# Kernel tuning notes

Hardware: AMD Instinct MI355X
Metric: run time of the kernel (lower is better)

The kernel has to match this reference:

```python
import jax, jax.numpy as jnp
import numpy as np

B, S, E, NH = 4, 1024, 512, 8
D = E // NH

def layer_norm(x, scale, bias, eps=1e-5):
    mu = jnp.mean(x, -1, keepdims=True)
    var = jnp.mean((x - mu) ** 2, -1, keepdims=True)
    return (x - mu) * jax.lax.rsqrt(var + eps) * scale + bias

def mha(qx, kx, vx, qw, qb, kw, kb, vw, vb, ow, ob, temp):
    b, sq, e = qx.shape
    sk = kx.shape[1]
    q = (qx @ qw + qb).reshape(b, sq, NH, D)
    k = (kx @ kw + kb).reshape(b, sk, NH, D)
    v = (vx @ vw + vb).reshape(b, sk, NH, D)
    scores = jnp.einsum('bqhd,bkhd->bhqk', q, k) * (D ** -0.5) / temp
    w = jax.nn.softmax(scores, axis=-1)  # dropout is identity in eval mode
    o = jnp.einsum('bhqk,bkhd->bqhd', w, v).reshape(b, sq, e)
    return o @ ow + ob

def setup_inputs():
    key = jax.random.key(0)
    ks = jax.random.split(key, 10)
    sc = 0.02  # init scale for weights
    return {
        'body_feats': jax.random.normal(ks[0], (B, S, E), jnp.float32),
        'limb_feats': jax.random.normal(ks[1], (B, S, E), jnp.float32),
        'attn_qw': jax.random.normal(ks[2], (4, E, E), jnp.float32) * sc,
        'attn_qb': jnp.zeros((4, E), jnp.float32),
        'attn_kw': jax.random.normal(ks[3], (4, E, E), jnp.float32) * sc,
        'attn_kb': jnp.zeros((4, E), jnp.float32),
        'attn_vw': jax.random.normal(ks[4], (4, E, E), jnp.float32) * sc,
        'attn_vb': jnp.zeros((4, E), jnp.float32),
        'attn_ow': jax.random.normal(ks[5], (4, E, E), jnp.float32) * sc,
        'attn_ob': jnp.zeros((4, E), jnp.float32),
        'ffn_w1': jax.random.normal(ks[6], (2, E, 4 * E), jnp.float32) * sc,
        'ffn_b1': jnp.zeros((2, 4 * E), jnp.float32),
        'ffn_w2': jax.random.normal(ks[7], (2, 4 * E, E), jnp.float32) * sc,
        'ffn_b2': jnp.zeros((2, E), jnp.float32),
        'norm_scale': jnp.ones((6, E), jnp.float32),
        'norm_bias': jnp.zeros((6, E), jnp.float32),
        'gate_w': jax.random.normal(ks[8], (2 * E, 2), jnp.float32) * sc,
        'gate_b': jnp.zeros((2,), jnp.float32),
        'temperature': 1,
    }

def reference(body_feats, limb_feats, attn_qw, attn_qb, attn_kw, attn_kb, attn_vw, attn_vb, attn_ow, attn_ob, ffn_w1, ffn_b1, ffn_w2, ffn_b2, norm_scale, norm_bias, gate_w, gate_b, temperature):
    temp = jnp.float32(temperature)
    # attn index: 0=self_body 1=self_limb 2=body2limb 3=limb2body
    # norm index: 0=norm1_body 1=norm2_body 2=norm3_body 3=norm1_limb 4=norm2_limb 5=norm3_limb
    def attn(i, qx, kx, vx):
        return mha(qx, kx, vx, attn_qw[i], attn_qb[i], attn_kw[i], attn_kb[i], attn_vw[i], attn_vb[i], attn_ow[i], attn_ob[i], temp)
    def ffn(i, x):
        return jax.nn.gelu(x @ ffn_w1[i] + ffn_b1[i], approximate=False) @ ffn_w2[i] + ffn_b2[i]
    def ln(i, x):
        return layer_norm(x, norm_scale[i], norm_bias[i])
    body = ln(0, body_feats + attn(0, body_feats, body_feats, body_feats))
    limb = ln(3, limb_feats + attn(1, limb_feats, limb_feats, limb_feats))
    body_cross = attn(2, body, limb, limb)
    limb_cross = attn(3, limb, body, body)
    body_gate = jax.nn.softmax(jnp.concatenate([body, body_cross], -1) @ gate_w + gate_b, axis=-1)
    limb_gate = jax.nn.softmax(jnp.concatenate([limb, limb_cross], -1) @ gate_w + gate_b, axis=-1)
    # NOTE: original torch code applies norm2_body to BOTH streams (preserved faithfully)
    body = ln(1, body * body_gate[..., 0:1] + body_cross * body_gate[..., 1:2])
    limb = ln(1, limb * limb_gate[..., 0:1] + limb_cross * limb_gate[..., 1:2])
    body = ln(2, body + ffn(0, body))
    limb = ln(5, limb + ffn(1, limb))
    return body, limb
```

## Files before the change

### kernel.cpp

```cpp
#include <hip/hip_runtime.h>

#define AS1 __attribute__((address_space(1)))
#define AS3 __attribute__((address_space(3)))

typedef __attribute__((ext_vector_type(4))) float f32x4;
typedef __attribute__((ext_vector_type(8))) short s16x8;

static __device__ __forceinline__ ushort f2bf(float f) {
  union { float f; unsigned u; } x; x.f = f;
  unsigned r = x.u + 0x7FFFu + ((x.u >> 16) & 1u);
  return (ushort)(r >> 16);
}
static __device__ __forceinline__ float bf2f(ushort u) {
  union { unsigned u; float f; } x; x.u = ((unsigned)u) << 16; return x.f;
}
static __device__ __forceinline__ float ex2(float x) {
  return __builtin_amdgcn_exp2f(x);
}
static __device__ __forceinline__ unsigned cvt_pk_bf16(float a, float b) {
  unsigned r;
  asm("v_cvt_pk_bf16_f32 %0, %1, %2" : "=v"(r) : "v"(a), "v"(b));
  return r;
}
static __device__ __forceinline__ float parse_scalar(const void* p) {
  int i = *(const int*)p;
  if (i > 0 && i < 1000000) return (float)i;
  union { int i; float f; } u; u.i = i; return u.f;
}

__global__ __launch_bounds__(256)
void transpose_all(const float* __restrict__ qw, const float* __restrict__ kw,
                   const float* __restrict__ vw, const float* __restrict__ ow,
                   const float* __restrict__ w1, const float* __restrict__ w2,
                   ushort* __restrict__ FW, ushort* __restrict__ WOT,
                   ushort* __restrict__ W1T, ushort* __restrict__ W2T)
{
  __shared__ float tile[32][33];
  int id = blockIdx.x;
  const float* in; ushort* out; int K, N, tx, ty;
  if (id < 3072) {
    int trip = id / 768, r = id - trip * 768, which = r >> 8, t2 = r & 255;
    int widx = (which == 0) ? trip : (trip ^ (trip >> 1));
    in = ((which == 0) ? qw : (which == 1) ? kw : vw) + (size_t)widx * 512 * 512;
    out = FW + (size_t)trip * 1536 * 512 + (size_t)which * 512 * 512;
    K = 512; N = 512; tx = t2 & 15; ty = t2 >> 4;
  } else if (id < 4096) {
    int r = id - 3072, wi = r >> 8, t2 = r & 255;
    in = ow + (size_t)wi * 512 * 512; out = WOT + (size_t)wi * 512 * 512;
    K = 512; N = 512; tx = t2 & 15; ty = t2 >> 4;
  } else if (id < 6144) {
    int r = id - 4096, s = r >> 10, t2 = r & 1023;
    in = w1 + (size_t)s * 512 * 2048; out = W1T + (size_t)s * 2048 * 512;
    K = 512; N = 2048; tx = t2 & 63; ty = t2 >> 6;
  } else {
    int r = id - 6144, s = r >> 10, t2 = r & 1023;
    in = w2 + (size_t)s * 2048 * 512; out = W2T + (size_t)s * 512 * 2048;
    K = 2048; N = 512; tx = t2 & 15; ty = t2 >> 4;
  }
  int nb = tx * 32, kb = ty * 32;
  int x = threadIdx.x, y = threadIdx.y;
  #pragma unroll
  for (int i = 0; i < 4; ++i)
    tile[y + i * 8][x] = in[(size_t)(kb + y + i * 8) * N + nb + x];
  __syncthreads();
  #pragma unroll
  for (int i = 0; i < 4; ++i)
    out[(size_t)(nb + y + i * 8) * K + kb + x] = f2bf(tile[x][y + i * 8]);
}

__global__ __launch_bounds__(256)
void cvt2_bf16(const float* __restrict__ a, const float* __restrict__ b,
               ushort* __restrict__ oa, ushort* __restrict__ ob)
{
  const float* in = blockIdx.y ? b : a;
  ushort* out = blockIdx.y ? ob : oa;
  int i = (blockIdx.x * 256 + threadIdx.x) * 4;
  float4 v = *(const float4*)(in + i);
  ushort4 o;
  o.x = f2bf(v.x); o.y = f2bf(v.y); o.z = f2bf(v.z); o.w = f2bf(v.w);
  *(ushort4*)(out + i) = o;
}

struct GemmArgs {
  const ushort* A; const ushort* Bt;
  const float *b0, *b1, *b2;
  float* outf; ushort* outb;
  ushort *qo, *ko, *vto;
  const void* sp;
  int M, N, K, kind;
};

template<int FM, int FN>
__global__ __launch_bounds__(256)
void gemm_k(GemmArgs g0, GemmArgs g1)
{
  constexpr int BM = FM * 32, BN = FN * 32;
  __shared__ ushort As[2][BM * 64];
  __shared__ ushort Bs[2][BN * 64];
  GemmArgs g = blockIdx.z ? g1 : g0;
  const int t = threadIdx.x, lane = t & 63, w = t >> 6;
  const int lr = lane & 15, gq = lane >> 4;
  const int wr = w >> 1, wc = w & 1;
  const int m0 = blockIdx.y * BM, n0 = blockIdx.x * BN;
  const int K = g.K;
  const int nk = K >> 6;

  auto stage = [&](int kt, int buf) {
    #pragma unroll
    for (int p = 0; p < FM; ++p) {
      int c = p * 256 + t, row = c >> 3, sl = c & 7;
      const ushort* src = g.A + (size_t)(m0 + row) * K + kt * 64 + ((sl ^ (row & 7)) << 3);
      __builtin_amdgcn_global_load_lds((const AS1 void*)src,
          (AS3 void*)(As[buf] + (size_t)(p * 256 + (t & ~63)) * 8), 16, 0, 0);
    }
    #pragma unroll
    for (int p = 0; p < FN; ++p) {
      int c = p * 256 + t, row = c >> 3, sl = c & 7;
      const ushort* src = g.Bt + (size_t)(n0 + row) * K + kt * 64 + ((sl ^ (row & 7)) << 3);
      __builtin_amdgcn_global_load_lds((const AS1 void*)src,
          (AS3 void*)(Bs[buf] + (size_t)(p * 256 + (t & ~63)) * 8), 16, 0, 0);
    }
  };

  f32x4 acc[FM][FN];
  f32x4 zero = {0.f, 0.f, 0.f, 0.f};
  #pragma unroll
  for (int m = 0; m < FM; ++m)
    #pragma unroll
    for (int n = 0; n < FN; ++n) acc[m][n] = zero;

  stage(0, 0);
  __syncthreads();
  for (int kt = 0; kt < nk; ++kt) {
    int cur = kt & 1;
    const ushort* Ab = As[cur];
    const ushort* Bb = Bs[cur];
    if (kt + 1 < nk) stage(kt + 1, cur ^ 1);
    #pragma unroll
    for (int ks = 0; ks < 2; ++ks) {
      s16x8 af[FM], bfv[FN];
      #pragma unroll
      for (int m = 0; m < FM; ++m) {
        int row = wr * (FM * 16) + m * 16 + lr;
        af[m] = *(const s16x8*)(Ab + row * 64 + (((ks * 4 + gq) ^ (row & 7)) << 3));
      }
      #pragma unroll
      for (int n = 0; n < FN; ++n) {
        int row = wc * (FN * 16) + n * 16 + lr;
        bfv[n] = *(const s16x8*)(Bb + row * 64 + (((ks * 4 + gq) ^ (row & 7)) << 3));
      }
      __builtin_amdgcn_s_setprio(1);
      #pragma unroll
      for (int m = 0; m < FM; ++m)
        #pragma unroll
        for (int n = 0; n < FN; ++n)
          acc[m][n] = __builtin_amdgcn_mfma_f32_16x16x32_bf16(af[m], bfv[n], acc[m][n], 0, 0, 0);
      __builtin_amdgcn_s_setprio(0);
    }
    __syncthreads();
  }

  float qs = 1.0f;
  if (g.kind == 3 && g.sp) qs = 0.125f / parse_scalar(g.sp) * 1.4426950408889634f;
  #pragma unroll
  for (int n = 0; n < FN; ++n) {
    int col = n0 + wc * (FN * 16) + n * 16 + lr;
    int seg = col >> 9, cm = col & 511;
    float bv;
    if (g.kind == 3) bv = (seg == 0) ? g.b0[cm] : (seg == 1) ? g.b1[cm] : g.b2[cm];
    else bv = g.b0 ? g.b0[col] : 0.f;
    #pragma unroll
    for (int m = 0; m < FM; ++m) {
      int rowb = m0 + wr * (FM * 16) + m * 16 + 4 * gq;
      if (g.kind == 3) {
        if (seg == 2) {
          int d = cm & 63, hh = cm >> 6, bb = rowb >> 10, s = rowb & 1023;
          ushort4 pk;
          pk.x = f2bf(acc[m][n][0] + bv); pk.y = f2bf(acc[m][n][1] + bv);
          pk.z = f2bf(acc[m][n][2] + bv); pk.w = f2bf(acc[m][n][3] + bv);
          *(ushort4*)(g.vto + (((size_t)(bb * 8 + hh) * 64 + d) << 10) + s) = pk;
        } else if (seg == 1) {
          #pragma unroll
          for (int r = 0; r < 4; ++r)
            g.ko[(size_t)(rowb + r) * 512 + cm] = f2bf(acc[m][n][r] + bv);
        } else {
          #pragma unroll
          for (int r = 0; r < 4; ++r)
            g.qo[(size_t)(rowb + r) * 512 + cm] = f2bf((acc[m][n][r] + bv) * qs);
        }
      } else {
        #pragma unroll
        for (int r = 0; r < 4; ++r) {
          float v = acc[m][n][r] + bv;
          if (g.kind == 2) v = 0.5f * v * (1.0f + erff(v * 0.70710678118654752f));
          if (g.kind == 0) g.outf[(size_t)(rowb + r) * g.N + col] = v;
          else g.outb[(size_t)(rowb + r) * g.N + col] = f2bf(v);
        }
      }
    }
  }
}

__global__ __launch_bounds__(256)
void attn_core(const ushort* __restrict__ Q0, const ushort* __restrict__ K0,
               const ushort* __restrict__ V0, ushort* __restrict__ O0,
               const ushort* __restrict__ Q1, const ushort* __restrict__ K1,
               const ushort* __restrict__ V1, ushort* __restrict__ O1)
{
  __shared__ ushort Ks[2][64 * 64];
  __shared__ ushort Vs[2][64 * 64];
  __shared__ ushort Ps[4][1024];
  const int str = blockIdx.y;
  const ushort* Q = str ? Q1 : Q0;
  const ushort* Kx = str ? K1 : K0;
  const ushort* VT = str ? V1 : V0;
  ushort* O = str ? O1 : O0;

  const int t = threadIdx.x, lane = t & 63, w = t >> 6;
  const int lr = lane & 15, g = lane >> 4;
  int bid = blockIdx.x;
  int L = (bid & 7) * 64 + (bid >> 3);
  int bh = L >> 4, qt = L & 15;
  size_t tbase = ((size_t)(bh >> 3) << 19) + ((size_t)(bh & 7) << 6);
  const ushort* Kbase = Kx + tbase;
  const ushort* Vbase = VT + ((size_t)bh << 16);
  int q0 = qt * 64 + w * 16;
  char* myPs = (char*)Ps[w];
  const int psw = (lr & 7) << 4;

  auto stage = [&](int kt, int buf) {
    #pragma unroll
    for (int p = 0; p < 2; ++p) {
      int c = p * 256 + t, row = c >> 3, sl = c & 7;
      const ushort* src = Kbase + (size_t)(kt * 64 + row) * 512 + ((sl ^ (row & 7)) << 3);
      __builtin_amdgcn_global_load_lds((const AS1 void*)src,
          (AS3 void*)(Ks[buf] + (size_t)(p * 256 + (t & ~63)) * 8), 16, 0, 0);
    }
    #pragma unroll
    for (int p = 0; p < 2; ++p) {
      int c = p * 256 + t, row = c >> 3, sl = c & 7;
      const ushort* src = Vbase + (size_t)row * 1024 + kt * 64 + ((sl ^ (row & 7)) << 3);
      __builtin_amdgcn_global_load_lds((const AS1 void*)src,
          (AS3 void*)(Vs[buf] + (size_t)(p * 256 + (t & ~63)) * 8), 16, 0, 0);
    }
  };

  s16x8 qf[2];
  #pragma unroll
  for (int ks = 0; ks < 2; ++ks)
    qf[ks] = *(const s16x8*)(Q + tbase + (size_t)(q0 + lr) * 512 + ks * 32 + g * 8);

  f32x4 po[4];
  f32x4 zero = {0.f, 0.f, 0.f, 0.f};
  #pragma unroll
  for (int dt = 0; dt < 4; ++dt) po[dt] = zero;
  float mrow = -1e30f, lsum = 0.f;

  stage(0, 0);
  __syncthreads();
  #pragma unroll 2
  for (int kt = 0; kt < 16; ++kt) {
    int cur = kt & 1;
    const ushort* Kb = Ks[cur];
    const ushort* Vb = Vs[cur];
    if (kt < 15) stage(kt + 1, cur ^ 1);

    f32x4 sc[4];
    #pragma unroll
    for (int c = 0; c < 4; ++c) {
      sc[c] = zero;
      #pragma unroll
      for (int ks = 0; ks < 2; ++ks) {
        int row = c * 16 + lr;
        s16x8 kf = *(const s16x8*)(Kb + row * 64 + (((ks * 4 + g) ^ (row & 7)) << 3));
        sc[c] = __builtin_amdgcn_mfma_f32_16x16x32_bf16(kf, qf[ks], sc[c], 0, 0, 0);
      }
    }

    float tm = sc[0][0];
    #pragma unroll
    for (int c = 0; c < 4; ++c)
      #pragma unroll
      for (int r = 0; r < 4; ++r) tm = fmaxf(tm, sc[c][r]);
    tm = fmaxf(tm, __shfl_xor(tm, 16));
    tm = fmaxf(tm, __shfl_xor(tm, 32));
    float nm = fmaxf(mrow, tm);
    float fr = ex2(mrow - nm);
    float ts = 0.f;
    #pragma unroll
    for (int c = 0; c < 4; ++c)
      #pragma unroll
      for (int r = 0; r < 4; ++r) {
        float pv = ex2(sc[c][r] - nm);
        sc[c][r] = pv;
        ts += pv;
      }
    ts += __shfl_xor(ts, 16);
    ts += __shfl_xor(ts, 32);
    lsum = lsum * fr + ts;
    mrow = nm;
    #pragma unroll
    for (int dt = 0; dt < 4; ++dt) po[dt] *= fr;

    #pragma unroll
    for (int c = 0; c < 4; ++c) {
      uint2 d;
      d.x = cvt_pk_bf16(sc[c][0], sc[c][1]);
      d.y = cvt_pk_bf16(sc[c][2], sc[c][3]);
      *(uint2*)(myPs + lr * 128 + ((c * 32 + g * 8) ^ psw)) = d;
    }
    s16x8 paf[2];
    #pragma unroll
    for (int ks = 0; ks < 2; ++ks)
      paf[ks] = *(const s16x8*)(myPs + lr * 128 + ((ks * 64 + g * 16) ^ psw));

    __builtin_amdgcn_s_setprio(1);
    #pragma unroll
    for (int dt = 0; dt < 4; ++dt) {
      int vrow = dt * 16 + lr;
      #pragma unroll
      for (int ks = 0; ks < 2; ++ks) {
        s16x8 vf = *(const s16x8*)(Vb + vrow * 64 + (((ks * 4 + g) ^ (vrow & 7)) << 3));
        po[dt] = __builtin_amdgcn_mfma_f32_16x16x32_bf16(vf, paf[ks], po[dt], 0, 0, 0);
      }
    }
    __builtin_amdgcn_s_setprio(0);
    __syncthreads();
  }

  float inv = 1.0f / lsum;
  #pragma unroll
  for (int dt = 0; dt < 4; ++dt) {
    ushort4 pk;
    pk.x = f2bf(po[dt][0] * inv);
    pk.y = f2bf(po[dt][1] * inv);
    pk.z = f2bf(po[dt][2] * inv);
    pk.w = f2bf(po[dt][3] * inv);
    *(ushort4*)(O + tbase + (size_t)(q0 + lr) * 512 + dt * 16 + 4 * g) = pk;
  }
}

__global__ __launch_bounds__(256)
void add_ln_ff2(const float* __restrict__ a0, const float* __restrict__ b0,
                ushort* __restrict__ o0, const float* __restrict__ a1,
                const float* __restrict__ b1, ushort* __restrict__ o1,
                const float* __restrict__ nsc, const float* __restrict__ nbi,
                int i0, int i1)
{
  const float* a = blockIdx.y ? a1 : a0;
  const float* b = blockIdx.y ? b1 : b0;
  ushort* outb = blockIdx.y ? o1 : o0;
  const float* scale = nsc + (blockIdx.y ? i1 : i0) * 512;
  const float* bias = nbi + (blockIdx.y ? i1 : i0) * 512;
  const int lane = threadIdx.x & 63, w = threadIdx.x >> 6;
  const size_t row = blockIdx.x * 4 + w;
  float x[8];
  #pragma unroll
  for (int j = 0; j < 8; j += 4) {
    float4 av = *(const float4*)(a + row * 512 + lane * 8 + j);
    float4 bv = *(const float4*)(b + row * 512 + lane * 8 + j);
    x[j] = av.x + bv.x; x[j + 1] = av.y + bv.y;
    x[j + 2] = av.z + bv.z; x[j + 3] = av.w + bv.w;
  }
  float s = 0.f, ss = 0.f;
  #pragma unroll
  for (int j = 0; j < 8; ++j) { s += x[j]; ss += x[j] * x[j]; }
  #pragma unroll
  for (int m = 1; m < 64; m <<= 1) { s += __shfl_xor(s, m); ss += __shfl_xor(ss, m); }
  float mu = s * (1.f / 512.f);
  float rstd = rsqrtf(ss * (1.f / 512.f) - mu * mu + 1e-5f);
  ushort o[8];
  #pragma unroll
  for (int j = 0; j < 8; ++j) {
    int e = lane * 8 + j;
    o[j] = f2bf((x[j] - mu) * rstd * scale[e] + bias[e]);
  }
  *(s16x8*)(outb + row * 512 + lane * 8) = *(s16x8*)o;
}

__global__ __launch_bounds__(256)
void add_ln_bf2(const ushort* __restrict__ a0, const float* __restrict__ b0,
                float* __restrict__ o0, const ushort* __restrict__ a1,
                const float* __restrict__ b1, float* __restrict__ o1,
                const float* __restrict__ nsc, const float* __restrict__ nbi,
                int i0, int i1)
{
  const ushort* a = blockIdx.y ? a1 : a0;
  const float* b = blockIdx.y ? b1 : b0;
  float* outf = blockIdx.y ? o1 : o0;
  const float* scale = nsc + (blockIdx.y ? i1 : i0) * 512;
  const float* bias = nbi + (blockIdx.y ? i1 : i0) * 512;
  const int lane = threadIdx.x & 63, w = threadIdx.x >> 6;
  const size_t row = blockIdx.x * 4 + w;
  s16x8 av = *(const s16x8*)(a + row * 512 + lane * 8);
  float x[8];
  #pragma unroll
  for (int j = 0; j < 8; j += 4) {
    float4 bv = *(const float4*)(b + row * 512 + lane * 8 + j);
    x[j] = bf2f((ushort)av[j]) + bv.x; x[j + 1] = bf2f((ushort)av[j + 1]) + bv.y;
    x[j + 2] = bf2f((ushort)av[j + 2]) + bv.z; x[j + 3] = bf2f((ushort)av[j + 3]) + bv.w;
  }
  float s = 0.f, ss = 0.f;
  #pragma unroll
  for (int j = 0; j < 8; ++j) { s += x[j]; ss += x[j] * x[j]; }
  #pragma unroll
  for (int m = 1; m < 64; m <<= 1) { s += __shfl_xor(s, m); ss += __shfl_xor(ss, m); }
  float mu = s * (1.f / 512.f);
  float rstd = rsqrtf(ss * (1.f / 512.f) - mu * mu + 1e-5f);
  float o[8];
  #pragma unroll
  for (int j = 0; j < 8; ++j) {
    int e = lane * 8 + j;
    o[j] = (x[j] - mu) * rstd * scale[e] + bias[e];
  }
  *(float4*)(outf + row * 512 + lane * 8) = *(float4*)o;
  *(float4*)(outf + row * 512 + lane * 8 + 4) = *(float4*)(o + 4);
}

__global__ __launch_bounds__(256)
void gate_ln2(const ushort* __restrict__ x0, const ushort* __restrict__ c0,
              ushort* __restrict__ o0, const ushort* __restrict__ x1,
              const ushort* __restrict__ c1, ushort* __restrict__ o1,
              const float* __restrict__ gw, const float* __restrict__ gb,
              const float* __restrict__ scale, const float* __restrict__ bias)
{
  const ushort* x = blockIdx.y ? x1 : x0;
  const ushort* cr = blockIdx.y ? c1 : c0;
  ushort* outb = blockIdx.y ? o1 : o0;
  const int lane = threadIdx.x & 63, w = threadIdx.x >> 6;
  const size_t row = blockIdx.x * 4 + w;
  s16x8 xv8 = *(const s16x8*)(x + row * 512 + lane * 8);
  s16x8 cv8 = *(const s16x8*)(cr + row * 512 + lane * 8);
  float xv[8], cv[8];
  #pragma unroll
  for (int j = 0; j < 8; ++j) { xv[j] = bf2f((ushort)xv8[j]); cv[j] = bf2f((ushort)cv8[j]); }
  float d0 = 0.f, d1 = 0.f;
  #pragma unroll
  for (int j = 0; j < 8; ++j) {
    int e = lane * 8 + j;
    float2 g0 = *(const float2*)(gw + 2 * e);
    float2 g1 = *(const float2*)(gw + 2 * (512 + e));
    d0 += xv[j] * g0.x + cv[j] * g1.x;
    d1 += xv[j] * g0.y + cv[j] * g1.y;
  }
  #pragma unroll
  for (int m = 1; m < 64; m <<= 1) { d0 += __shfl_xor(d0, m); d1 += __shfl_xor(d1, m); }
  d0 += gb[0]; d1 += gb[1];
  float mx = fmaxf(d0, d1);
  float e0 = __expf(d0 - mx), e1 = __expf(d1 - mx);
  float inv = 1.0f / (e0 + e1);
  float g0w = e0 * inv, g1w = e1 * inv;
  float xc[8];
  float s = 0.f, ss = 0.f;
  #pragma unroll
  for (int j = 0; j < 8; ++j) {
    xc[j] = xv[j] * g0w + cv[j] * g1w;
    s += xc[j]; ss += xc[j] * xc[j];
  }
  #pragma unroll
  for (int m = 1; m < 64; m <<= 1) { s += __shfl_xor(s, m); ss += __shfl_xor(ss, m); }
  float mu = s * (1.f / 512.f);
  float rstd = rsqrtf(ss * (1.f / 512.f) - mu * mu + 1e-5f);
  ushort o[8];
  #pragma unroll
  for (int j = 0; j < 8; ++j) {
    int e = lane * 8 + j;
    o[j] = f2bf((xc[j] - mu) * rstd * scale[e] + bias[e]);
  }
  *(s16x8*)(outb + row * 512 + lane * 8) = *(s16x8*)o;
}

extern "C" void kernel_launch(void* const* d_in, const int* in_sizes, int n_in,
                              void* d_out, int out_size, void* d_ws, size_t ws_size,
                              hipStream_t stream)
{
  (void)in_sizes; (void)n_in; (void)out_size; (void)ws_size;
  const int T = 4096, E = 512, HD = 2048;
  const float* body = (const float*)d_in[0];
  const float* limb = (const float*)d_in[1];
  const float* qw = (const float*)d_in[2];  const float* qb = (const float*)d_in[3];
  const float* kw = (const float*)d_in[4];  const float* kb = (const float*)d_in[5];
  const float* vw = (const float*)d_in[6];  const float* vb = (const float*)d_in[7];
  const float* ow = (const float*)d_in[8];  const float* ob = (const float*)d_in[9];
  const float* w1 = (const float*)d_in[10]; const float* fb1 = (const float*)d_in[11];
  const float* w2 = (const float*)d_in[12]; const float* fb2 = (const float*)d_in[13];
  const float* nsc = (const float*)d_in[14]; const float* nbi = (const float*)d_in[15];
  const float* gw = (const float*)d_in[16];  const float* gb = (const float*)d_in[17];
  const void* temp = d_in[18];

  char* ws = (char*)d_ws;
  size_t off = 0;
  auto alloc = [&](size_t b) { char* p = ws + off; off += (b + 255) & ~(size_t)255; return p; };
  ushort* FW    = (ushort*)alloc((size_t)4 * 1536 * 512 * 2);
  ushort* WOT   = (ushort*)alloc((size_t)4 * E * E * 2);
  ushort* W1T   = (ushort*)alloc((size_t)2 * E * HD * 2);
  ushort* W2T   = (ushort*)alloc((size_t)2 * HD * E * 2);
  ushort* XB    = (ushort*)alloc((size_t)T * E * 2);
  ushort* XL    = (ushort*)alloc((size_t)T * E * 2);
  float*  PROJA = (float*)alloc((size_t)T * E * 4);
  float*  PROJB = (float*)alloc((size_t)T * E * 4);
  ushort* BODYb = (ushort*)alloc((size_t)T * E * 2);
  ushort* LIMBb = (ushort*)alloc((size_t)T * E * 2);
  ushort* BCRb  = (ushort*)alloc((size_t)T * E * 2);
  ushort* LCRb  = (ushort*)alloc((size_t)T * E * 2);
  ushort* GBb   = (ushort*)alloc((size_t)T * E * 2);
  ushort* GLb   = (ushort*)alloc((size_t)T * E * 2);
  ushort* QA    = (ushort*)alloc((size_t)T * E * 2);
  ushort* KA    = (ushort*)alloc((size_t)T * E * 2);
  ushort* VTA   = (ushort*)alloc((size_t)T * E * 2);
  ushort* QB    = (ushort*)alloc((size_t)T * E * 2);
  ushort* KB    = (ushort*)alloc((size_t)T * E * 2);
  ushort* VTB   = (ushort*)alloc((size_t)T * E * 2);
  ushort* AOA   = (ushort*)alloc((size_t)T * E * 2);
  ushort* AOB   = (ushort*)alloc((size_t)T * E * 2);
  ushort* H1A   = QA;
  ushort* H1B   = KB;
  float*  FFNA  = PROJA;
  float*  FFNB  = PROJB;

  transpose_all<<<8192, dim3(32, 8), 0, stream>>>(qw, kw, vw, ow, w1, w2, FW, WOT, W1T, W2T);
  cvt2_bf16<<<dim3(T * E / 1024, 2), 256, 0, stream>>>(body, limb, XB, XL);

  auto qkv_pair = [&](const ushort* A0, int t0, ushort* q0, ushort* k0, ushort* v0,
                      const ushort* A1, int t1, ushort* q1, ushort* k1, ushort* v1) {
    GemmArgs a{}, b{};
    int kv0 = t0 ^ (t0 >> 1), kv1 = t1 ^ (t1 >> 1);
    a.A = A0; a.Bt = FW + (size_t)t0 * 1536 * 512;
    a.b0 = qb + t0 * E; a.b1 = kb + kv0 * E; a.b2 = vb + kv0 * E;
    a.qo = q0; a.ko = k0; a.vto = v0; a.sp = temp; a.M = T; a.N = 1536; a.K = E; a.kind = 3;
    b = a;
    b.A = A1; b.Bt = FW + (size_t)t1 * 1536 * 512;
    b.b0 = qb + t1 * E; b.b1 = kb + kv1 * E; b.b2 = vb + kv1 * E;
    b.qo = q1; b.ko = k1; b.vto = v1;
    gemm_k<4, 4><<<dim3(12, 32, 2), 256, 0, stream>>>(a, b);
  };
  auto oproj_pair = [&](const ushort* A0, int i0, float* of0, ushort* ob0,
                        const ushort* A1, int i1, float* of1, ushort* ob1, int kind) {
    GemmArgs a{}, b{};
    a.A = A0; a.Bt = WOT + (size_t)i0 * E * E; a.b0 = ob + i0 * E;
    a.outf = of0; a.outb = ob0; a.M = T; a.N = E; a.K = E; a.kind = kind;
    b = a;
    b.A = A1; b.Bt = WOT + (size_t)i1 * E * E; b.b0 = ob + i1 * E;
    b.outf = of1; b.outb = ob1;
    gemm_k<2, 4><<<dim3(4, 64, 2), 256, 0, stream>>>(a, b);
  };

  qkv_pair(XB, 0, QA, KA, VTA, XL, 1, QB, KB, VTB);
  attn_core<<<dim3(512, 2), 256, 0, stream>>>(QA, KA, VTA, AOA, QB, KB, VTB, AOB);
  oproj_pair(AOA, 0, PROJA, nullptr, AOB, 1, PROJB, nullptr, 0);
  add_ln_ff2<<<dim3(T / 4, 2), 256, 0, stream>>>(body, PROJA, BODYb, limb, PROJB, LIMBb,
                                                 nsc, nbi, 0, 3);
  qkv_pair(BODYb, 2, QA, KA, VTA, LIMBb, 3, QB, KB, VTB);
  attn_core<<<dim3(512, 2), 256, 0, stream>>>(QA, KB, VTB, AOA, QB, KA, VTA, AOB);
  oproj_pair(AOA, 2, nullptr, BCRb, AOB, 3, nullptr, LCRb, 1);

  gate_ln2<<<dim3(T / 4, 2), 256, 0, stream>>>(BODYb, BCRb, GBb, LIMBb, LCRb, GLb,
                                               gw, gb, nsc + E, nbi + E);

  {
    GemmArgs a{}, b{};
    a.A = GBb; a.Bt = W1T; a.b0 = fb1; a.outb = H1A;
    a.M = T; a.N = HD; a.K = E; a.kind = 2;
    b = a; b.A = GLb; b.Bt = W1T + (size_t)HD * E; b.b0 = fb1 + HD; b.outb = H1B;
    gemm_k<4, 4><<<dim3(16, 32, 2), 256, 0, stream>>>(a, b);
  }
  {
    GemmArgs a{}, b{};
    a.A = H1A; a.Bt = W2T; a.b0 = fb2; a.outf = FFNA;
    a.M = T; a.N = E; a.K = HD; a.kind = 0;
    b = a; b.A = H1B; b.Bt = W2T + (size_t)HD * E; b.b0 = fb2 + E; b.outf = FFNB;
    gemm_k<2, 4><<<dim3(4, 64, 2), 256, 0, stream>>>(a, b);
  }
  add_ln_bf2<<<dim3(T / 4, 2), 256, 0, stream>>>(GBb, FFNA, (float*)d_out,
                                                 GLb, FFNB, (float*)d_out + (size_t)T * E,
                                                 nsc, nbi, 2, 5);
}
```

Baseline: 404.1 us.

## Use tanh GELU, bf16 intermediates, merged input conversion, smaller output GEMM tiles

The exact erf GELU becomes a tanh-form approximation built from exp2 and rcp. The output-projection and FFN2 GEMMs now write bf16 instead of fp32, and the add+layernorm kernels read bf16. The fp32-to-bf16 input conversion is folded into the weight transpose launch as extra blocks. The N=512 GEMMs switch from 2x4 to 2x2 fragment tiles with twice the grid, and together these aim to cut launches, memory traffic and erf cost at some accuracy risk.

```diff
diff --git a/kernel.cpp b/kernel.cpp
--- a/kernel.cpp
+++ b/kernel.cpp
@@ -22,6 +22,12 @@
   asm("v_cvt_pk_bf16_f32 %0, %1, %2" : "=v"(r) : "v"(a), "v"(b));
   return r;
 }
+static __device__ __forceinline__ float gelu_fast(float v) {
+  float u = 0.7978845608028654f * (v + 0.044715f * v * v * v);
+  float e = ex2(u * 2.885390081777927f);
+  float r = __builtin_amdgcn_rcpf(e + 1.0f);
+  return v - v * r;
+}
 static __device__ __forceinline__ float parse_scalar(const void* p) {
   int i = *(const int*)p;
   if (i > 0 && i < 1000000) return (float)i;
@@ -32,11 +38,26 @@
 void transpose_all(const float* __restrict__ qw, const float* __restrict__ kw,
                    const float* __restrict__ vw, const float* __restrict__ ow,
                    const float* __restrict__ w1, const float* __restrict__ w2,
+                   const float* __restrict__ body, const float* __restrict__ limb,
                    ushort* __restrict__ FW, ushort* __restrict__ WOT,
-                   ushort* __restrict__ W1T, ushort* __restrict__ W2T)
+                   ushort* __restrict__ W1T, ushort* __restrict__ W2T,
+                   ushort* __restrict__ XB, ushort* __restrict__ XL)
 {
   __shared__ float tile[32][33];
   int id = blockIdx.x;
+  if (id >= 8192) {
+    int id2 = id - 8192;
+    const float* in = (id2 >= 2048) ? limb : body;
+    ushort* out = (id2 >= 2048) ? XL : XB;
+    int j = id2 & 2047;
+    int t = threadIdx.y * 32 + threadIdx.x;
+    int i = (j * 256 + t) * 4;
+    float4 v = *(const float4*)(in + i);
+    ushort4 o;
+    o.x = f2bf(v.x); o.y = f2bf(v.y); o.z = f2bf(v.z); o.w = f2bf(v.w);
+    *(ushort4*)(out + i) = o;
+    return;
+  }
   const float* in; ushort* out; int K, N, tx, ty;
   if (id < 3072) {
     int trip = id / 768, r = id - trip * 768, which = r >> 8, t2 = r & 255;
@@ -66,19 +87,6 @@
   #pragma unroll
   for (int i = 0; i < 4; ++i)
     out[(size_t)(nb + y + i * 8) * K + kb + x] = f2bf(tile[x][y + i * 8]);
-}
-
-__global__ __launch_bounds__(256)
-void cvt2_bf16(const float* __restrict__ a, const float* __restrict__ b,
-               ushort* __restrict__ oa, ushort* __restrict__ ob)
-{
-  const float* in = blockIdx.y ? b : a;
-  ushort* out = blockIdx.y ? ob : oa;
-  int i = (blockIdx.x * 256 + threadIdx.x) * 4;
-  float4 v = *(const float4*)(in + i);
-  ushort4 o;
-  o.x = f2bf(v.x); o.y = f2bf(v.y); o.z = f2bf(v.z); o.w = f2bf(v.w);
-  *(ushort4*)(out + i) = o;
 }
 
 struct GemmArgs {
@@ -192,7 +200,7 @@
         #pragma unroll
         for (int r = 0; r < 4; ++r) {
           float v = acc[m][n][r] + bv;
-          if (g.kind == 2) v = 0.5f * v * (1.0f + erff(v * 0.70710678118654752f));
+          if (g.kind == 2) v = gelu_fast(v);
           if (g.kind == 0) g.outf[(size_t)(rowb + r) * g.N + col] = v;
           else g.outb[(size_t)(rowb + r) * g.N + col] = f2bf(v);
         }
@@ -341,26 +349,28 @@
 }
 
 __global__ __launch_bounds__(256)
-void add_ln_ff2(const float* __restrict__ a0, const float* __restrict__ b0,
+void add_ln_fb2(const float* __restrict__ a0, const ushort* __restrict__ b0,
                 ushort* __restrict__ o0, const float* __restrict__ a1,
-                const float* __restrict__ b1, ushort* __restrict__ o1,
+                const ushort* __restrict__ b1, ushort* __restrict__ o1,
                 const float* __restrict__ nsc, const float* __restrict__ nbi,
                 int i0, int i1)
 {
   const float* a = blockIdx.y ? a1 : a0;
-  const float* b = blockIdx.y ? b1 : b0;
+  const ushort* b = blockIdx.y ? b1 : b0;
   ushort* outb = blockIdx.y ? o1 : o0;
   const float* scale = nsc + (blockIdx.y ? i1 : i0) * 512;
   const float* bias = nbi + (blockIdx.y ? i1 : i0) * 512;
   const int lane = threadIdx.x & 63, w = threadIdx.x >> 6;
   const size_t row = blockIdx.x * 4 + w;
+  s16x8 bv8 = *(const s16x8*)(b + row * 512 + lane * 8);
   float x[8];
   #pragma unroll
   for (int j = 0; j < 8; j += 4) {
     float4 av = *(const float4*)(a + row * 512 + lane * 8 + j);
-    float4 bv = *(const float4*)(b + row * 512 + lane * 8 + j);
-    x[j] = av.x + bv.x; x[j + 1] = av.y + bv.y;
-    x[j + 2] = av.z + bv.z; x[j + 3] = av.w + bv.w;
+    x[j] = av.x + bf2f((ushort)bv8[j]);
+    x[j + 1] = av.y + bf2f((ushort)bv8[j + 1]);
+    x[j + 2] = av.z + bf2f((ushort)bv8[j + 2]);
+    x[j + 3] = av.w + bf2f((ushort)bv8[j + 3]);
   }
   float s = 0.f, ss = 0.f;
   #pragma unroll
@@ -379,27 +389,25 @@
 }
 
 __global__ __launch_bounds__(256)
-void add_ln_bf2(const ushort* __restrict__ a0, const float* __restrict__ b0,
+void add_ln_bb2(const ushort* __restrict__ a0, const ushort* __restrict__ b0,
                 float* __restrict__ o0, const ushort* __restrict__ a1,
-                const float* __restrict__ b1, float* __restrict__ o1,
+                const ushort* __restrict__ b1, float* __restrict__ o1,
                 const float* __restrict__ nsc, const float* __restrict__ nbi,
                 int i0, int i1)
 {
   const ushort* a = blockIdx.y ? a1 : a0;
-  const float* b = blockIdx.y ? b1 : b0;
+  const ushort* b = blockIdx.y ? b1 : b0;
   float* outf = blockIdx.y ? o1 : o0;
   const float* scale = nsc + (blockIdx.y ? i1 : i0) * 512;
   const float* bias = nbi + (blockIdx.y ? i1 : i0) * 512;
   const int lane = threadIdx.x & 63, w = threadIdx.x >> 6;
   const size_t row = blockIdx.x * 4 + w;
   s16x8 av = *(const s16x8*)(a + row * 512 + lane * 8);
+  s16x8 bv = *(const s16x8*)(b + row * 512 + lane * 8);
   float x[8];
   #pragma unroll
-  for (int j = 0; j < 8; j += 4) {
-    float4 bv = *(const float4*)(b + row * 512 + lane * 8 + j);
-    x[j] = bf2f((ushort)av[j]) + bv.x; x[j + 1] = bf2f((ushort)av[j + 1]) + bv.y;
-    x[j + 2] = bf2f((ushort)av[j + 2]) + bv.z; x[j + 3] = bf2f((ushort)av[j + 3]) + bv.w;
-  }
+  for (int j = 0; j < 8; ++j)
+    x[j] = bf2f((ushort)av[j]) + bf2f((ushort)bv[j]);
   float s = 0.f, ss = 0.f;
   #pragma unroll
   for (int j = 0; j < 8; ++j) { s += x[j]; ss += x[j] * x[j]; }
@@ -497,8 +505,8 @@
   ushort* W2T   = (ushort*)alloc((size_t)2 * HD * E * 2);
   ushort* XB    = (ushort*)alloc((size_t)T * E * 2);
   ushort* XL    = (ushort*)alloc((size_t)T * E * 2);
-  float*  PROJA = (float*)alloc((size_t)T * E * 4);
-  float*  PROJB = (float*)alloc((size_t)T * E * 4);
+  ushort* PROJA = (ushort*)alloc((size_t)T * E * 2);
+  ushort* PROJB = (ushort*)alloc((size_t)T * E * 2);
   ushort* BODYb = (ushort*)alloc((size_t)T * E * 2);
   ushort* LIMBb = (ushort*)alloc((size_t)T * E * 2);
   ushort* BCRb  = (ushort*)alloc((size_t)T * E * 2);
@@ -515,11 +523,11 @@
   ushort* AOB   = (ushort*)alloc((size_t)T * E * 2);
   ushort* H1A   = QA;
   ushort* H1B   = KB;
-  float*  FFNA  = PROJA;
-  float*  FFNB  = PROJB;
-
-  transpose_all<<<8192, dim3(32, 8), 0, stream>>>(qw, kw, vw, ow, w1, w2, FW, WOT, W1T, W2T);
-  cvt2_bf16<<<dim3(T * E / 1024, 2), 256, 0, stream>>>(body, limb, XB, XL);
+  ushort* F2A   = PROJA;
+  ushort* F2B   = PROJB;
+
+  transpose_all<<<12288, dim3(32, 8), 0, stream>>>(qw, kw, vw, ow, w1, w2, body, limb,
+                                                   FW, WOT, W1T, W2T, XB, XL);
 
   auto qkv_pair = [&](const ushort* A0, int t0, ushort* q0, ushort* k0, ushort* v0,
                       const ushort* A1, int t1, ushort* q1, ushort* k1, ushort* v1) {
@@ -534,25 +542,25 @@
     b.qo = q1; b.ko = k1; b.vto = v1;
     gemm_k<4, 4><<<dim3(12, 32, 2), 256, 0, stream>>>(a, b);
   };
-  auto oproj_pair = [&](const ushort* A0, int i0, float* of0, ushort* ob0,
-                        const ushort* A1, int i1, float* of1, ushort* ob1, int kind) {
+  auto oproj_pair = [&](const ushort* A0, int i0, ushort* ob0,
+                        const ushort* A1, int i1, ushort* ob1) {
     GemmArgs a{}, b{};
     a.A = A0; a.Bt = WOT + (size_t)i0 * E * E; a.b0 = ob + i0 * E;
-    a.outf = of0; a.outb = ob0; a.M = T; a.N = E; a.K = E; a.kind = kind;
+    a.outb = ob0; a.M = T; a.N = E; a.K = E; a.kind = 1;
     b = a;
     b.A = A1; b.Bt = WOT + (size_t)i1 * E * E; b.b0 = ob + i1 * E;
-    b.outf = of1; b.outb = ob1;
-    gemm_k<2, 4><<<dim3(4, 64, 2), 256, 0, stream>>>(a, b);
+    b.outb = ob1;
+    gemm_k<2, 2><<<dim3(8, 64, 2), 256, 0, stream>>>(a, b);
   };
 
   qkv_pair(XB, 0, QA, KA, VTA, XL, 1, QB, KB, VTB);
   attn_core<<<dim3(512, 2), 256, 0, stream>>>(QA, KA, VTA, AOA, QB, KB, VTB, AOB);
-  oproj_pair(AOA, 0, PROJA, nullptr, AOB, 1, PROJB, nullptr, 0);
-  add_ln_ff2<<<dim3(T / 4, 2), 256, 0, stream>>>(body, PROJA, BODYb, limb, PROJB, LIMBb,
+  oproj_pair(AOA, 0, PROJA, AOB, 1, PROJB);
+  add_ln_fb2<<<dim3(T / 4, 2), 256, 0, stream>>>(body, PROJA, BODYb, limb, PROJB, LIMBb,
                                                  nsc, nbi, 0, 3);
   qkv_pair(BODYb, 2, QA, KA, VTA, LIMBb, 3, QB, KB, VTB);
   attn_core<<<dim3(512, 2), 256, 0, stream>>>(QA, KB, VTB, AOA, QB, KA, VTA, AOB);
-  oproj_pair(AOA, 2, nullptr, BCRb, AOB, 3, nullptr, LCRb, 1);
+  oproj_pair(AOA, 2, BCRb, AOB, 3, LCRb);
 
   gate_ln2<<<dim3(T / 4, 2), 256, 0, stream>>>(BODYb, BCRb, GBb, LIMBb, LCRb, GLb,
                                                gw, gb, nsc + E, nbi + E);
@@ -566,12 +574,12 @@
   }
   {
     GemmArgs a{}, b{};
-    a.A = H1A; a.Bt = W2T; a.b0 = fb2; a.outf = FFNA;
-    a.M = T; a.N = E; a.K = HD; a.kind = 0;
-    b = a; b.A = H1B; b.Bt = W2T + (size_t)HD * E; b.b0 = fb2 + E; b.outf = FFNB;
-    gemm_k<2, 4><<<dim3(4, 64, 2), 256, 0, stream>>>(a, b);
-  }
-  add_ln_bf2<<<dim3(T / 4, 2), 256, 0, stream>>>(GBb, FFNA, (float*)d_out,
-                                                 GLb, FFNB, (float*)d_out + (size_t)T * E,
+    a.A = H1A; a.Bt = W2T; a.b0 = fb2; a.outb = F2A;
+    a.M = T; a.N = E; a.K = HD; a.kind = 1;
+    b = a; b.A = H1B; b.Bt = W2T + (size_t)HD * E; b.b0 = fb2 + E; b.outb = F2B;
+    gemm_k<2, 2><<<dim3(8, 64, 2), 256, 0, stream>>>(a, b);
+  }
+  add_ln_bb2<<<dim3(T / 4, 2), 256, 0, stream>>>(GBb, F2A, (float*)d_out,
+                                                 GLb, F2B, (float*)d_out + (size_t)T * E,
                                                  nsc, nbi, 2, 5);
 }
```

Result: faster. 377.4 us (-6.6%).
